# Optimization experiments

Measured on AMD Instinct MI355X. Metric: run time of the kernel, lower is better.

Reference implementation:

```python
import jax, jax.numpy as jnp
import numpy as np

THETA = 0.5  # forward default arg
ALPHA = 0.2  # LeakyReLU negative slope
NEG_INF = -9e15


def setup_inputs() -> dict:
    key = jax.random.key(0)
    k1, k2, k3, k4, k5 = jax.random.split(key, 5)
    N, F_IN, F_OUT = 8192, 256, 256
    h = jax.random.normal(k1, (N, F_IN), dtype=jnp.float32)
    adj = jax.random.randint(k2, (N, N), 0, 2, dtype=jnp.int32)
    cv_values = jax.random.uniform(k3, (N,), dtype=jnp.float32)
    # xavier_uniform with gain=1.414
    g = 1.414
    bw = g * np.sqrt(6.0 / (F_IN + F_OUT))
    W = jax.random.uniform(k4, (F_IN, F_OUT), dtype=jnp.float32, minval=-bw, maxval=bw)
    ba = g * np.sqrt(6.0 / (2 * F_OUT + 1))
    a = jax.random.uniform(k5, (2 * F_OUT, 1), dtype=jnp.float32, minval=-ba, maxval=ba)
    return {"h": h, "adj": adj, "cv_values": cv_values, "W": W, "a": a}


def reference(h, adj, cv_values, W, a):
    # Wh: [N, F_out]
    Wh = h @ W
    F_out = Wh.shape[1]
    a1 = a[:F_out, 0]   # [F_out]
    a2 = a[F_out:, 0]   # [F_out]
    # e_ij = LeakyReLU([Wh_i ; Wh_j] . a) = LeakyReLU(Wh_i.a1 + Wh_j.a2)
    f1 = Wh @ a1        # [N]
    f2 = Wh @ a2        # [N]
    e = jax.nn.leaky_relu(f1[:, None] + f2[None, :], negative_slope=ALPHA)
    # CV bias: theta * cv_i broadcast across row i
    e = e + THETA * cv_values[:, None]
    att = jnp.where(adj > 0, e, jnp.float32(NEG_INF))
    att = jax.nn.softmax(att, axis=1)
    # dropout is identity in eval mode (training=False)
    h_prime = att @ Wh  # [N, F_out]
    return jax.nn.elu(h_prime)  # concat=True branch
```

## Files before the change

kernel.cpp:

```cpp
#include <hip/hip_runtime.h>
#include <cstdint>
#include <cstddef>

typedef _Float16 half8 __attribute__((ext_vector_type(8)));
typedef _Float16 half4 __attribute__((ext_vector_type(4)));
typedef float f32x4 __attribute__((ext_vector_type(4)));
typedef int iv4 __attribute__((ext_vector_type(4)));

#define GAT_N 8192
#define GAT_F 256
#define GAT_NQ 8
#define GAT_ALPHA 0.2f
#define GAT_LOG2E 1.4426950408889634f

__device__ inline unsigned enc_f32(float x) {
    unsigned b = __float_as_uint(x);
    return (b & 0x80000000u) ? ~b : (b | 0x80000000u);
}
__device__ inline float dec_f32(unsigned u) {
    unsigned b = (u & 0x80000000u) ? (u ^ 0x80000000u) : ~u;
    return __uint_as_float(b);
}

__device__ inline unsigned pack8(iv4 v0, iv4 v1) {
    return (unsigned)(v0[0] > 0)        | ((unsigned)(v0[1] > 0) << 1)
         | ((unsigned)(v0[2] > 0) << 2) | ((unsigned)(v0[3] > 0) << 3)
         | ((unsigned)(v1[0] > 0) << 4) | ((unsigned)(v1[1] > 0) << 5)
         | ((unsigned)(v1[2] > 0) << 6) | ((unsigned)(v1[3] > 0) << 7);
}


__global__ __launch_bounds__(256) void gat_k0b_convert(
    const float* __restrict__ W, _Float16* __restrict__ WT,
    unsigned* __restrict__ f2mxEnc)
{
    const int g = blockIdx.x * 256 + threadIdx.x;
    if (g == 0) *f2mxEnc = 0u;
    const int k = g >> 8, n = g & 255;
    WT[n * GAT_F + k] = (_Float16)W[g];
}

__global__ __launch_bounds__(256, 2) void gat_k1_gemm(
    const float* __restrict__ h, const _Float16* __restrict__ WT,
    const float* __restrict__ a, _Float16* __restrict__ whT2,
    float* __restrict__ f1L, float* __restrict__ f2L,
    unsigned* __restrict__ f2mxEnc)
{
    __shared__ float sP1[4][16], sP2[4][16];
    const int wv = threadIdx.x >> 6;
    const int lane = threadIdx.x & 63;
    const int l15 = lane & 15;
    const int quad = lane >> 4;
    const int r0 = blockIdx.x * 16;

    f32x4 acc[4];
    #pragma unroll
    for (int t = 0; t < 4; ++t) { f32x4 z = {0.f,0.f,0.f,0.f}; acc[t] = z; }

    #pragma unroll
    for (int k0 = 0; k0 < GAT_F; k0 += 32) {
        const float* ap = h + (size_t)(r0 + l15) * GAT_F + k0 + quad * 8;
        const float4 a0 = *reinterpret_cast<const float4*>(ap);
        const float4 a1 = *reinterpret_cast<const float4*>(ap + 4);
        half8 af;
        af[0] = (_Float16)a0.x; af[1] = (_Float16)a0.y;
        af[2] = (_Float16)a0.z; af[3] = (_Float16)a0.w;
        af[4] = (_Float16)a1.x; af[5] = (_Float16)a1.y;
        af[6] = (_Float16)a1.z; af[7] = (_Float16)a1.w;
        #pragma unroll
        for (int t = 0; t < 4; ++t) {
            half8 bf = *reinterpret_cast<const half8*>(
                WT + (size_t)(wv * 64 + t * 16 + l15) * GAT_F + k0 + quad * 8);
            acc[t] = __builtin_amdgcn_mfma_f32_16x16x32_f16(af, bf, acc[t], 0, 0, 0);
        }
    }

    float p1[4] = {0.f,0.f,0.f,0.f}, p2[4] = {0.f,0.f,0.f,0.f};
    #pragma unroll
    for (int t = 0; t < 4; ++t) {
        float a1c = a[wv * 64 + t * 16 + l15];
        float a2c = a[GAT_F + wv * 64 + t * 16 + l15];
        #pragma unroll
        for (int r = 0; r < 4; ++r) {
            p1[r] = fmaf(acc[t][r], a1c, p1[r]);
            p2[r] = fmaf(acc[t][r], a2c, p2[r]);
        }
    }
    #pragma unroll
    for (int off = 1; off < 16; off <<= 1) {
        #pragma unroll
        for (int r = 0; r < 4; ++r) {
            p1[r] += __shfl_xor(p1[r], off);
            p2[r] += __shfl_xor(p2[r], off);
        }
    }
    if (l15 == 0) {
        #pragma unroll
        for (int r = 0; r < 4; ++r) {
            sP1[wv][quad * 4 + r] = p1[r];
            sP2[wv][quad * 4 + r] = p2[r];
        }
    }
    __syncthreads();
    if (threadIdx.x < 16) {
        const int row = threadIdx.x;
        const float s1 = (sP1[0][row] + sP1[1][row] + sP1[2][row] + sP1[3][row]) * GAT_LOG2E;
        const float s2 = (sP2[0][row] + sP2[1][row] + sP2[2][row] + sP2[3][row]) * GAT_LOG2E;
        f1L[r0 + row] = s1;
        f2L[r0 + row] = s2;
        float mx = s2;
        #pragma unroll
        for (int off = 1; off < 16; off <<= 1) mx = fmaxf(mx, __shfl_xor(mx, off));
        if (row == 0) atomicMax(f2mxEnc, enc_f32(mx));
    }

    const size_t tbase = (size_t)(r0 >> 6) * 16384
                       + (((r0 & 63) >> 3) + (quad >> 1)) * 2048
                       + (quad & 1) * 4;
    #pragma unroll
    for (int t = 0; t < 4; ++t) {
        const int c = wv * 64 + t * 16 + l15;
        half4 hv;
        #pragma unroll
        for (int r = 0; r < 4; ++r) hv[r] = (_Float16)acc[t][r];
        *reinterpret_cast<half4*>(whT2 + tbase + c * 8) = hv;
    }
}

__global__ __launch_bounds__(256, 2) void gat_k3_attn(
    const int* __restrict__ adj, const float* __restrict__ f1L,
    const float* __restrict__ f2L, const unsigned* __restrict__ f2mxEnc,
    const _Float16* __restrict__ whT2,
    _Float16* __restrict__ Ph,
    float* __restrict__ L)
{
    const int bx = blockIdx.x;
    const int q  = bx & 7;
    const int rb = bx >> 3;
    const int wv = threadIdx.x >> 6;
    const int lane = threadIdx.x & 63;
    const int l15 = lane & 15;
    const int quad = lane >> 4;

    const int kq = q * 1024;
    const int r0 = rb * 128 + wv * 32;
    const int rA = r0 + l15;
    const int rB = rA + 16;

    const float fmxL = dec_f32(*f2mxEnc);
    const float f1A = f1L[rA];
    const float f1B = f1L[rB];
    const float sA = f1A + fmxL;
    const float sBv = f1B + fmxL;
    const float CA = fmaxf(sA, GAT_ALPHA * sA);
    const float CB = fmaxf(sBv, GAT_ALPHA * sBv);
    const float uA = f1A - CA, vA = GAT_ALPHA * f1A - CA;
    const float uB = f1B - CB, vB = GAT_ALPHA * f1B - CB;

    f32x4 acc[2][16];
    #pragma unroll
    for (int s = 0; s < 2; ++s)
        #pragma unroll
        for (int t = 0; t < 16; ++t) {
            f32x4 z = {0.f,0.f,0.f,0.f};
            acc[s][t] = z;
        }
    float d0 = 0.f, d1 = 0.f;

    const int* aprA = adj + (size_t)rA * GAT_N + kq + quad * 8;
    const int* aprB = adj + (size_t)rB * GAT_N + kq + quad * 8;
    const float* f2q = f2L + kq + quad * 8;

    const _Float16* bfp0 = whT2 + (size_t)(q * 16) * 16384
                         + (size_t)quad * 2048 + (size_t)l15 * 8;

    iv4 xA0, xA1, xA2, xA3, xB0, xB1, xB2, xB3;
    #define ADJLOAD(s)                                                         \
        {                                                                      \
            const iv4* pa = reinterpret_cast<const iv4*>(aprA + (s) * 64);     \
            const iv4* pb = reinterpret_cast<const iv4*>(aprB + (s) * 64);     \
            xA0 = __builtin_nontemporal_load(pa);                              \
            xA1 = __builtin_nontemporal_load(pa + 1);                          \
            xA2 = __builtin_nontemporal_load(pa + 8);                          \
            xA3 = __builtin_nontemporal_load(pa + 9);                          \
            xB0 = __builtin_nontemporal_load(pb);                              \
            xB1 = __builtin_nontemporal_load(pb + 1);                          \
            xB2 = __builtin_nontemporal_load(pb + 8);                          \
            xB3 = __builtin_nontemporal_load(pb + 9);                          \
        }
    #define ADJPACK(ma, mb)                                                    \
        {                                                                      \
            ma = pack8(xA0, xA1) | (pack8(xA2, xA3) << 8);                     \
            mb = pack8(xB0, xB1) | (pack8(xB2, xB3) << 8);                     \
        }

    ADJLOAD(0)
    float4 nfa = *reinterpret_cast<const float4*>(f2q);
    float4 nfb = *reinterpret_cast<const float4*>(f2q + 4);
    unsigned cmA, cmB;
    ADJPACK(cmA, cmB)
    unsigned nmA = 0, nmB = 0;

    for (int step = 0; step < 16; ++step) {
        if (step < 15) ADJLOAD(step + 1)
        const _Float16* bstep = bfp0 + (size_t)step * 16384;

        #pragma unroll
        for (int k2 = 0; k2 < 2; ++k2) {
            const int u = step * 2 + k2;
            const float4 cfa = nfa, cfb = nfb;
            if (u < 31) {
                nfa = *reinterpret_cast<const float4*>(f2q + (u + 1) * 32);
                nfb = *reinterpret_cast<const float4*>(f2q + (u + 1) * 32 + 4);
            }
            const unsigned mA = (cmA >> (k2 * 8)) & 0xffu;
            const unsigned mB = (cmB >> (k2 * 8)) & 0xffu;
            const float f2v[8] = {cfa.x, cfa.y, cfa.z, cfa.w,
                                  cfb.x, cfb.y, cfb.z, cfb.w};
            float af2[8];
            #pragma unroll
            for (int j = 0; j < 8; ++j) af2[j] = GAT_ALPHA * f2v[j];

            half8 pA, pB;
            #pragma unroll
            for (int j = 0; j < 8; ++j) {
                float pa = __builtin_amdgcn_exp2f(fmaxf(uA + f2v[j], vA + af2[j]));
                pa = (mA & (1u << j)) ? pa : 0.f;
                d0 += pa;
                pA[j] = (_Float16)pa;
                float pb = __builtin_amdgcn_exp2f(fmaxf(uB + f2v[j], vB + af2[j]));
                pb = (mB & (1u << j)) ? pb : 0.f;
                d1 += pb;
                pB[j] = (_Float16)pb;
            }

            const _Float16* bk = bstep + k2 * 8192;
            #pragma unroll
            for (int t = 0; t < 16; ++t) {
                half8 bf = *reinterpret_cast<const half8*>(bk + t * 128);
                acc[0][t] = __builtin_amdgcn_mfma_f32_16x16x32_f16(pA, bf, acc[0][t], 0, 0, 0);
                acc[1][t] = __builtin_amdgcn_mfma_f32_16x16x32_f16(pB, bf, acc[1][t], 0, 0, 0);
            }
        }
        if (step < 15) ADJPACK(nmA, nmB)
        cmA = nmA; cmB = nmB;
    }
    #undef ADJLOAD
    #undef ADJPACK

    d0 += __shfl_xor(d0, 16); d0 += __shfl_xor(d0, 32);
    d1 += __shfl_xor(d1, 16); d1 += __shfl_xor(d1, 32);
    if (lane < 16) {
        float* Lq = L + q * GAT_N;
        Lq[rA] = d0; Lq[rB] = d1;
    }

    const int wid = rb * 4 + wv;
    _Float16* Pq = Ph + ((size_t)q * 256 + wid) * 8192;
    #pragma unroll
    for (int s = 0; s < 2; ++s)
        #pragma unroll
        for (int t = 0; t < 16; ++t) {
            half4 hv;
            #pragma unroll
            for (int r = 0; r < 4; ++r) hv[r] = (_Float16)acc[s][t][r];
            __builtin_nontemporal_store(hv,
                reinterpret_cast<half4*>(Pq + (size_t)(((s * 16 + t) * 64 + lane) * 4)));
        }
}

__global__ __launch_bounds__(256) void gat_k4_final(
    const _Float16* __restrict__ Ph, const float* __restrict__ L,
    float* __restrict__ out)
{
    const int tid = threadIdx.x;
    const int wid = blockIdx.x >> 3;
    __shared__ float s_rl[32];
    if (tid < 32) {
        const int row = wid * 32 + tid;
        float s = 0.f;
        #pragma unroll
        for (int q = 0; q < GAT_NQ; ++q) s += L[q * GAT_N + row];
        s_rl[tid] = 1.0f / fmaxf(s, 1e-30f);
    }
    __syncthreads();

    const int idx = blockIdx.x * 256 + tid;
    const int rem = idx & 2047;
    const int lane = rem & 63;
    const int st = rem >> 6;
    const int s = st >> 4, t = st & 15;
    const int l15 = lane & 15, quad = lane >> 4;
    const int lrow0 = s * 16 + quad * 4;
    const int col = t * 16 + l15;

    float accv[4] = {0.f, 0.f, 0.f, 0.f};
    #pragma unroll
    for (int q = 0; q < GAT_NQ; ++q) {
        half4 v = __builtin_nontemporal_load(reinterpret_cast<const half4*>(
            Ph + ((size_t)q * 256 + wid) * 8192 + (size_t)rem * 4));
        #pragma unroll
        for (int r = 0; r < 4; ++r) accv[r] += (float)v[r];
    }
    #pragma unroll
    for (int r = 0; r < 4; ++r) {
        const float v = accv[r] * s_rl[lrow0 + r];
        const float o = v > 0.f ? v : expm1f(v);
        __builtin_nontemporal_store(o,
            &out[(size_t)(wid * 32 + lrow0 + r) * GAT_F + col]);
    }
}

extern "C" void kernel_launch(void* const* d_in, const int* in_sizes, int n_in,
                              void* d_out, int out_size, void* d_ws, size_t ws_size,
                              hipStream_t stream)
{
    const float* h   = (const float*)d_in[0];
    const int*   adj = (const int*)d_in[1];
    const float* W   = (const float*)d_in[3];
    const float* a   = (const float*)d_in[4];
    float* out = (float*)d_out;
    char* ws = (char*)d_ws;

    const size_t SLAB = (size_t)GAT_N * GAT_F * 2;

    size_t off = 0;
    _Float16* whT2 = (_Float16*)(ws + off); off += SLAB;
    _Float16* Ph  = (_Float16*)(ws + off); off += GAT_NQ * SLAB;
    _Float16* WT  = (_Float16*)(ws + off); off += (size_t)GAT_F * GAT_F * 2;
    float* f1L = (float*)(ws + off); off += GAT_N * 4;
    float* f2L = (float*)(ws + off); off += GAT_N * 4;
    float* L   = (float*)(ws + off); off += GAT_NQ * GAT_N * 4;
    unsigned* f2mxEnc = (unsigned*)(ws + off); off += 256;

    gat_k0b_convert<<<256, 256, 0, stream>>>(W, WT, f2mxEnc);
    gat_k1_gemm<<<512, 256, 0, stream>>>(h, WT, a, whT2, f1L, f2L, f2mxEnc);
    gat_k3_attn<<<512, 256, 0, stream>>>(adj, f1L, f2L, f2mxEnc, whT2, Ph, L);
    gat_k4_final<<<2048, 256, 0, stream>>>(Ph, L, out);
}
```

Baseline: 470.5 us.

## Stage Wh tiles through double-buffered LDS and cache f2 slice in shared memory

The attention kernel now cooperatively loads each step's 32 KB fp16 Wh tile from global memory into a double-buffered LDS array. It overlaps the next tile's global load with the current step's MFMA work, and the four waves read B fragments from LDS instead of each fetching them from global/L2. The f2 slice for the block is cached in LDS, and MFMA sections get raised wave priority via s_setprio. Nontemporal hints are dropped in the reduction kernel. The cost is 64 KB+ of LDS per block, which may cut occupancy below the 2 blocks requested by launch bounds, plus a __syncthreads each step.

```diff
diff --git a/kernel.cpp b/kernel.cpp
--- a/kernel.cpp
+++ b/kernel.cpp
@@ -134,6 +134,9 @@
     _Float16* __restrict__ Ph,
     float* __restrict__ L)
 {
+    __shared__ __align__(16) _Float16 sB[2][16384];
+    __shared__ __align__(16) float sF2[1024];
+
     const int bx = blockIdx.x;
     const int q  = bx & 7;
     const int rb = bx >> 3;
@@ -150,13 +153,18 @@
     const float fmxL = dec_f32(*f2mxEnc);
     const float f1A = f1L[rA];
     const float f1B = f1L[rB];
-    const float sA = f1A + fmxL;
+    const float sAv = f1A + fmxL;
     const float sBv = f1B + fmxL;
-    const float CA = fmaxf(sA, GAT_ALPHA * sA);
+    const float CA = fmaxf(sAv, GAT_ALPHA * sAv);
     const float CB = fmaxf(sBv, GAT_ALPHA * sBv);
     const float uA = f1A - CA, vA = GAT_ALPHA * f1A - CA;
     const float uB = f1B - CB, vB = GAT_ALPHA * f1B - CB;
 
+    {
+        const float4 v = *reinterpret_cast<const float4*>(f2L + kq + threadIdx.x * 4);
+        *reinterpret_cast<float4*>(&sF2[threadIdx.x * 4]) = v;
+    }
+
     f32x4 acc[2][16];
     #pragma unroll
     for (int s = 0; s < 2; ++s)
@@ -169,10 +177,6 @@
 
     const int* aprA = adj + (size_t)rA * GAT_N + kq + quad * 8;
     const int* aprB = adj + (size_t)rB * GAT_N + kq + quad * 8;
-    const float* f2q = f2L + kq + quad * 8;
-
-    const _Float16* bfp0 = whT2 + (size_t)(q * 16) * 16384
-                         + (size_t)quad * 2048 + (size_t)l15 * 8;
 
     iv4 xA0, xA1, xA2, xA3, xB0, xB1, xB2, xB3;
     #define ADJLOAD(s)                                                         \
@@ -194,57 +198,106 @@
             mb = pack8(xB0, xB1) | (pack8(xB2, xB3) << 8);                     \
         }
 
+    const _Float16* tile0 = whT2 + (size_t)(q * 16) * 16384
+                          + (size_t)wv * 4096 + (size_t)lane * 8;
+    _Float16* const lbase0 = &sB[0][wv * 4096 + lane * 8];
+    int4 g0, g1, g2, g3, g4, g5, g6, g7;
+    #define STAGE_LOAD(step)                                                   \
+        {                                                                      \
+            const _Float16* gp = tile0 + (size_t)(step) * 16384;               \
+            g0 = *reinterpret_cast<const int4*>(gp);                           \
+            g1 = *reinterpret_cast<const int4*>(gp + 512);                     \
+            g2 = *reinterpret_cast<const int4*>(gp + 1024);                    \
+            g3 = *reinterpret_cast<const int4*>(gp + 1536);                    \
+            g4 = *reinterpret_cast<const int4*>(gp + 2048);                    \
+            g5 = *reinterpret_cast<const int4*>(gp + 2560);                    \
+            g6 = *reinterpret_cast<const int4*>(gp + 3072);                    \
+            g7 = *reinterpret_cast<const int4*>(gp + 3584);                    \
+        }
+    #define STAGE_WRITE(buf)                                                   \
+        {                                                                      \
+            _Float16* lp = lbase0 + (buf) * 16384;                             \
+            *reinterpret_cast<int4*>(lp)        = g0;                          \
+            *reinterpret_cast<int4*>(lp + 512)  = g1;                          \
+            *reinterpret_cast<int4*>(lp + 1024) = g2;                          \
+            *reinterpret_cast<int4*>(lp + 1536) = g3;                          \
+            *reinterpret_cast<int4*>(lp + 2048) = g4;                          \
+            *reinterpret_cast<int4*>(lp + 2560) = g5;                          \
+            *reinterpret_cast<int4*>(lp + 3072) = g6;                          \
+            *reinterpret_cast<int4*>(lp + 3584) = g7;                          \
+        }
+
+    unsigned cmA, cmB, nmA, nmB;
+    const _Float16* const sflat = &sB[0][0];
+
+    #define STEP_COMPUTE(cur, step)                                            \
+        {                                                                      \
+            _Pragma("unroll")                                                  \
+            for (int k2 = 0; k2 < 2; ++k2) {                                   \
+                const float* fp = &sF2[(step) * 64 + k2 * 32 + quad * 8];      \
+                const float4 cfa = *reinterpret_cast<const float4*>(fp);       \
+                const float4 cfb = *reinterpret_cast<const float4*>(fp + 4);   \
+                const unsigned mA = (cmA >> (k2 * 8)) & 0xffu;                 \
+                const unsigned mB = (cmB >> (k2 * 8)) & 0xffu;                 \
+                const float f2v[8] = {cfa.x, cfa.y, cfa.z, cfa.w,              \
+                                      cfb.x, cfb.y, cfb.z, cfb.w};             \
+                float af2[8];                                                  \
+                _Pragma("unroll")                                              \
+                for (int j = 0; j < 8; ++j) af2[j] = GAT_ALPHA * f2v[j];       \
+                half8 pA, pB;                                                  \
+                _Pragma("unroll")                                              \
+                for (int j = 0; j < 8; ++j) {                                  \
+                    float pa = __builtin_amdgcn_exp2f(                         \
+                        fmaxf(uA + f2v[j], vA + af2[j]));                      \
+                    pa = (mA & (1u << j)) ? pa : 0.f;                          \
+                    d0 += pa;                                                  \
+                    pA[j] = (_Float16)pa;                                      \
+                    float pb = __builtin_amdgcn_exp2f(                         \
+                        fmaxf(uB + f2v[j], vB + af2[j]));                      \
+                    pb = (mB & (1u << j)) ? pb : 0.f;                          \
+                    d1 += pb;                                                  \
+                    pB[j] = (_Float16)pb;                                      \
+                }                                                              \
+                const _Float16* bk = sflat + (cur) * 16384                     \
+                                   + (k2 * 4 + quad) * 2048 + l15 * 8;         \
+                __builtin_amdgcn_s_setprio(1);                                 \
+                _Pragma("unroll")                                              \
+                for (int t = 0; t < 16; ++t) {                                 \
+                    half8 bf = *reinterpret_cast<const half8*>(bk + t * 128);  \
+                    acc[0][t] = __builtin_amdgcn_mfma_f32_16x16x32_f16(        \
+                        pA, bf, acc[0][t], 0, 0, 0);                           \
+                    acc[1][t] = __builtin_amdgcn_mfma_f32_16x16x32_f16(        \
+                        pB, bf, acc[1][t], 0, 0, 0);                           \
+                }                                                              \
+                __builtin_amdgcn_s_setprio(0);                                 \
+            }                                                                  \
+        }
+
+    STAGE_LOAD(0)
     ADJLOAD(0)
-    float4 nfa = *reinterpret_cast<const float4*>(f2q);
-    float4 nfb = *reinterpret_cast<const float4*>(f2q + 4);
-    unsigned cmA, cmB;
+    STAGE_WRITE(0)
     ADJPACK(cmA, cmB)
-    unsigned nmA = 0, nmB = 0;
+    __syncthreads();
 
     for (int step = 0; step < 16; ++step) {
-        if (step < 15) ADJLOAD(step + 1)
-        const _Float16* bstep = bfp0 + (size_t)step * 16384;
-
-        #pragma unroll
-        for (int k2 = 0; k2 < 2; ++k2) {
-            const int u = step * 2 + k2;
-            const float4 cfa = nfa, cfb = nfb;
-            if (u < 31) {
-                nfa = *reinterpret_cast<const float4*>(f2q + (u + 1) * 32);
-                nfb = *reinterpret_cast<const float4*>(f2q + (u + 1) * 32 + 4);
-            }
-            const unsigned mA = (cmA >> (k2 * 8)) & 0xffu;
-            const unsigned mB = (cmB >> (k2 * 8)) & 0xffu;
-            const float f2v[8] = {cfa.x, cfa.y, cfa.z, cfa.w,
-                                  cfb.x, cfb.y, cfb.z, cfb.w};
-            float af2[8];
-            #pragma unroll
-            for (int j = 0; j < 8; ++j) af2[j] = GAT_ALPHA * f2v[j];
-
-            half8 pA, pB;
-            #pragma unroll
-            for (int j = 0; j < 8; ++j) {
-                float pa = __builtin_amdgcn_exp2f(fmaxf(uA + f2v[j], vA + af2[j]));
-                pa = (mA & (1u << j)) ? pa : 0.f;
-                d0 += pa;
-                pA[j] = (_Float16)pa;
-                float pb = __builtin_amdgcn_exp2f(fmaxf(uB + f2v[j], vB + af2[j]));
-                pb = (mB & (1u << j)) ? pb : 0.f;
-                d1 += pb;
-                pB[j] = (_Float16)pb;
-            }
-
-            const _Float16* bk = bstep + k2 * 8192;
-            #pragma unroll
-            for (int t = 0; t < 16; ++t) {
-                half8 bf = *reinterpret_cast<const half8*>(bk + t * 128);
-                acc[0][t] = __builtin_amdgcn_mfma_f32_16x16x32_f16(pA, bf, acc[0][t], 0, 0, 0);
-                acc[1][t] = __builtin_amdgcn_mfma_f32_16x16x32_f16(pB, bf, acc[1][t], 0, 0, 0);
-            }
-        }
-        if (step < 15) ADJPACK(nmA, nmB)
-        cmA = nmA; cmB = nmB;
-    }
+        const int cur = step & 1;
+        if (step < 15) {
+            STAGE_LOAD(step + 1)
+            ADJLOAD(step + 1)
+        }
+
+        STEP_COMPUTE(cur, step)
+
+        if (step < 15) {
+            STAGE_WRITE(1 - cur)
+            ADJPACK(nmA, nmB)
+            cmA = nmA; cmB = nmB;
+            __syncthreads();
+        }
+    }
+    #undef STAGE_LOAD
+    #undef STAGE_WRITE
+    #undef STEP_COMPUTE
     #undef ADJLOAD
     #undef ADJPACK
 
@@ -297,8 +350,8 @@
     float accv[4] = {0.f, 0.f, 0.f, 0.f};
     #pragma unroll
     for (int q = 0; q < GAT_NQ; ++q) {
-        half4 v = __builtin_nontemporal_load(reinterpret_cast<const half4*>(
-            Ph + ((size_t)q * 256 + wid) * 8192 + (size_t)rem * 4));
+        half4 v = *reinterpret_cast<const half4*>(
+            Ph + ((size_t)q * 256 + wid) * 8192 + (size_t)rem * 4);
         #pragma unroll
         for (int r = 0; r < 4; ++r) accv[r] += (float)v[r];
     }
@@ -306,8 +359,7 @@
     for (int r = 0; r < 4; ++r) {
         const float v = accv[r] * s_rl[lrow0 + r];
         const float o = v > 0.f ? v : expm1f(v);
-        __builtin_nontemporal_store(o,
-            &out[(size_t)(wid * 32 + lrow0 + r) * GAT_F + col]);
+        out[(size_t)(wid * 32 + lrow0 + r) * GAT_F + col] = o;
     }
 }
 
```

After: 607.2 us. +29.0%, slower.

## Stage Wh tiles in LDS with async double buffering, halve rows per wave

Applied to the files above, without the earlier changes.

The attention kernel now loads each 32-column K-slice of Wh into shared memory through global_load_lds into a double buffer, and all four waves share it instead of each reading B fragments from global memory. Each wave now handles 16 rows instead of 32, so the grid doubles to 1024 blocks. Launch bounds rise to 4 blocks per CU, and f2 values are cached in LDS. The intent is less redundant global B traffic and higher occupancy, at the cost of a barrier every step and half the MFMA reuse per B fragment. The final reduction kernel and the partial-result layout are adjusted to match the 16-row tiles, and the adj loads drop their nontemporal hint.

```diff
diff --git a/kernel.cpp b/kernel.cpp
--- a/kernel.cpp
+++ b/kernel.cpp
@@ -127,13 +127,16 @@
     }
 }
 
-__global__ __launch_bounds__(256, 2) void gat_k3_attn(
+__global__ __launch_bounds__(256, 4) void gat_k3_attn(
     const int* __restrict__ adj, const float* __restrict__ f1L,
     const float* __restrict__ f2L, const unsigned* __restrict__ f2mxEnc,
     const _Float16* __restrict__ whT2,
     _Float16* __restrict__ Ph,
     float* __restrict__ L)
 {
+    __shared__ __align__(16) _Float16 sB[2][8192];
+    __shared__ __align__(16) float sF2[1024];
+
     const int bx = blockIdx.x;
     const int q  = bx & 7;
     const int rb = bx >> 3;
@@ -143,130 +146,115 @@
     const int quad = lane >> 4;
 
     const int kq = q * 1024;
-    const int r0 = rb * 128 + wv * 32;
+    const int r0 = rb * 64 + wv * 16;
     const int rA = r0 + l15;
-    const int rB = rA + 16;
 
     const float fmxL = dec_f32(*f2mxEnc);
     const float f1A = f1L[rA];
-    const float f1B = f1L[rB];
-    const float sA = f1A + fmxL;
-    const float sBv = f1B + fmxL;
-    const float CA = fmaxf(sA, GAT_ALPHA * sA);
-    const float CB = fmaxf(sBv, GAT_ALPHA * sBv);
+    const float sAv = f1A + fmxL;
+    const float CA = fmaxf(sAv, GAT_ALPHA * sAv);
     const float uA = f1A - CA, vA = GAT_ALPHA * f1A - CA;
-    const float uB = f1B - CB, vB = GAT_ALPHA * f1B - CB;
-
-    f32x4 acc[2][16];
-    #pragma unroll
-    for (int s = 0; s < 2; ++s)
-        #pragma unroll
-        for (int t = 0; t < 16; ++t) {
-            f32x4 z = {0.f,0.f,0.f,0.f};
-            acc[s][t] = z;
-        }
-    float d0 = 0.f, d1 = 0.f;
+
+    {
+        const float4 v = *reinterpret_cast<const float4*>(f2L + kq + threadIdx.x * 4);
+        *reinterpret_cast<float4*>(&sF2[threadIdx.x * 4]) = v;
+    }
+
+    f32x4 acc[16];
+    #pragma unroll
+    for (int t = 0; t < 16; ++t) { f32x4 z = {0.f,0.f,0.f,0.f}; acc[t] = z; }
+    float d0 = 0.f;
 
     const int* aprA = adj + (size_t)rA * GAT_N + kq + quad * 8;
-    const int* aprB = adj + (size_t)rB * GAT_N + kq + quad * 8;
-    const float* f2q = f2L + kq + quad * 8;
-
-    const _Float16* bfp0 = whT2 + (size_t)(q * 16) * 16384
-                         + (size_t)quad * 2048 + (size_t)l15 * 8;
-
-    iv4 xA0, xA1, xA2, xA3, xB0, xB1, xB2, xB3;
+
+    iv4 xA0, xA1;
     #define ADJLOAD(s)                                                         \
         {                                                                      \
-            const iv4* pa = reinterpret_cast<const iv4*>(aprA + (s) * 64);     \
-            const iv4* pb = reinterpret_cast<const iv4*>(aprB + (s) * 64);     \
-            xA0 = __builtin_nontemporal_load(pa);                              \
-            xA1 = __builtin_nontemporal_load(pa + 1);                          \
-            xA2 = __builtin_nontemporal_load(pa + 8);                          \
-            xA3 = __builtin_nontemporal_load(pa + 9);                          \
-            xB0 = __builtin_nontemporal_load(pb);                              \
-            xB1 = __builtin_nontemporal_load(pb + 1);                          \
-            xB2 = __builtin_nontemporal_load(pb + 8);                          \
-            xB3 = __builtin_nontemporal_load(pb + 9);                          \
-        }
-    #define ADJPACK(ma, mb)                                                    \
+            const int* pa = aprA + (s) * 32;                                   \
+            xA0 = *reinterpret_cast<const iv4*>(pa);                           \
+            xA1 = *reinterpret_cast<const iv4*>(pa + 4);                       \
+        }
+    #define ADJPACK(m) { m = pack8(xA0, xA1); }
+
+    const _Float16* tile0 = whT2 + (size_t)(q * 32) * 8192
+                          + wv * 2048 + (size_t)lane * 8;
+    #define STAGE(buf, step)                                                   \
         {                                                                      \
-            ma = pack8(xA0, xA1) | (pack8(xA2, xA3) << 8);                     \
-            mb = pack8(xB0, xB1) | (pack8(xB2, xB3) << 8);                     \
-        }
-
+            _Pragma("unroll")                                                  \
+            for (int i = 0; i < 4; ++i) {                                      \
+                const _Float16* gp = tile0 + (size_t)(step) * 8192 + i * 512;  \
+                _Float16* lp = &sB[buf][wv * 2048 + i * 512];                  \
+                __builtin_amdgcn_global_load_lds(                              \
+                    (const __attribute__((address_space(1))) void*)gp,         \
+                    (__attribute__((address_space(3))) void*)lp, 16, 0, 0);    \
+            }                                                                  \
+        }
+
+    unsigned cmA, nmA;
     ADJLOAD(0)
-    float4 nfa = *reinterpret_cast<const float4*>(f2q);
-    float4 nfb = *reinterpret_cast<const float4*>(f2q + 4);
-    unsigned cmA, cmB;
-    ADJPACK(cmA, cmB)
-    unsigned nmA = 0, nmB = 0;
-
-    for (int step = 0; step < 16; ++step) {
-        if (step < 15) ADJLOAD(step + 1)
-        const _Float16* bstep = bfp0 + (size_t)step * 16384;
-
-        #pragma unroll
-        for (int k2 = 0; k2 < 2; ++k2) {
-            const int u = step * 2 + k2;
-            const float4 cfa = nfa, cfb = nfb;
-            if (u < 31) {
-                nfa = *reinterpret_cast<const float4*>(f2q + (u + 1) * 32);
-                nfb = *reinterpret_cast<const float4*>(f2q + (u + 1) * 32 + 4);
-            }
-            const unsigned mA = (cmA >> (k2 * 8)) & 0xffu;
-            const unsigned mB = (cmB >> (k2 * 8)) & 0xffu;
-            const float f2v[8] = {cfa.x, cfa.y, cfa.z, cfa.w,
-                                  cfb.x, cfb.y, cfb.z, cfb.w};
-            float af2[8];
-            #pragma unroll
-            for (int j = 0; j < 8; ++j) af2[j] = GAT_ALPHA * f2v[j];
-
-            half8 pA, pB;
-            #pragma unroll
-            for (int j = 0; j < 8; ++j) {
-                float pa = __builtin_amdgcn_exp2f(fmaxf(uA + f2v[j], vA + af2[j]));
-                pa = (mA & (1u << j)) ? pa : 0.f;
-                d0 += pa;
-                pA[j] = (_Float16)pa;
-                float pb = __builtin_amdgcn_exp2f(fmaxf(uB + f2v[j], vB + af2[j]));
-                pb = (mB & (1u << j)) ? pb : 0.f;
-                d1 += pb;
-                pB[j] = (_Float16)pb;
-            }
-
-            const _Float16* bk = bstep + k2 * 8192;
-            #pragma unroll
-            for (int t = 0; t < 16; ++t) {
-                half8 bf = *reinterpret_cast<const half8*>(bk + t * 128);
-                acc[0][t] = __builtin_amdgcn_mfma_f32_16x16x32_f16(pA, bf, acc[0][t], 0, 0, 0);
-                acc[1][t] = __builtin_amdgcn_mfma_f32_16x16x32_f16(pB, bf, acc[1][t], 0, 0, 0);
-            }
-        }
-        if (step < 15) ADJPACK(nmA, nmB)
-        cmA = nmA; cmB = nmB;
-    }
+    STAGE(0, 0)
+    ADJPACK(cmA)
+    __syncthreads();
+
+    const _Float16* const sflat = &sB[0][0];
+
+    for (int step = 0; step < 32; ++step) {
+        const int cur = step & 1;
+        if (step < 31) {
+            ADJLOAD(step + 1)
+            STAGE(1 - cur, step + 1)
+        }
+
+        const float* fp = &sF2[step * 32 + quad * 8];
+        const float4 cfa = *reinterpret_cast<const float4*>(fp);
+        const float4 cfb = *reinterpret_cast<const float4*>(fp + 4);
+        const float f2v[8] = {cfa.x, cfa.y, cfa.z, cfa.w,
+                              cfb.x, cfb.y, cfb.z, cfb.w};
+        float af2[8];
+        #pragma unroll
+        for (int j = 0; j < 8; ++j) af2[j] = GAT_ALPHA * f2v[j];
+
+        half8 pA;
+        #pragma unroll
+        for (int j = 0; j < 8; ++j) {
+            float pa = __builtin_amdgcn_exp2f(fmaxf(uA + f2v[j], vA + af2[j]));
+            pa = (cmA & (1u << j)) ? pa : 0.f;
+            d0 += pa;
+            pA[j] = (_Float16)pa;
+        }
+
+        const _Float16* bk = sflat + cur * 8192 + quad * 2048 + l15 * 8;
+        __builtin_amdgcn_s_setprio(1);
+        #pragma unroll
+        for (int t = 0; t < 16; ++t) {
+            half8 bf = *reinterpret_cast<const half8*>(bk + t * 128);
+            acc[t] = __builtin_amdgcn_mfma_f32_16x16x32_f16(pA, bf, acc[t], 0, 0, 0);
+        }
+        __builtin_amdgcn_s_setprio(0);
+
+        if (step < 31) {
+            ADJPACK(nmA)
+            cmA = nmA;
+            __syncthreads();
+        }
+    }
+    #undef STAGE
     #undef ADJLOAD
     #undef ADJPACK
 
     d0 += __shfl_xor(d0, 16); d0 += __shfl_xor(d0, 32);
-    d1 += __shfl_xor(d1, 16); d1 += __shfl_xor(d1, 32);
-    if (lane < 16) {
-        float* Lq = L + q * GAT_N;
-        Lq[rA] = d0; Lq[rB] = d1;
-    }
+    if (lane < 16) L[q * GAT_N + rA] = d0;
 
     const int wid = rb * 4 + wv;
-    _Float16* Pq = Ph + ((size_t)q * 256 + wid) * 8192;
-    #pragma unroll
-    for (int s = 0; s < 2; ++s)
-        #pragma unroll
-        for (int t = 0; t < 16; ++t) {
-            half4 hv;
-            #pragma unroll
-            for (int r = 0; r < 4; ++r) hv[r] = (_Float16)acc[s][t][r];
-            __builtin_nontemporal_store(hv,
-                reinterpret_cast<half4*>(Pq + (size_t)(((s * 16 + t) * 64 + lane) * 4)));
-        }
+    _Float16* Pq = Ph + ((size_t)q * 512 + wid) * 4096;
+    #pragma unroll
+    for (int t = 0; t < 16; ++t) {
+        half4 hv;
+        #pragma unroll
+        for (int r = 0; r < 4; ++r) hv[r] = (_Float16)acc[t][r];
+        __builtin_nontemporal_store(hv,
+            reinterpret_cast<half4*>(Pq + (size_t)((t * 64 + lane) * 4)));
+    }
 }
 
 __global__ __launch_bounds__(256) void gat_k4_final(
@@ -274,10 +262,10 @@
     float* __restrict__ out)
 {
     const int tid = threadIdx.x;
-    const int wid = blockIdx.x >> 3;
-    __shared__ float s_rl[32];
-    if (tid < 32) {
-        const int row = wid * 32 + tid;
+    const int wid = blockIdx.x >> 2;
+    __shared__ float s_rl[16];
+    if (tid < 16) {
+        const int row = wid * 16 + tid;
         float s = 0.f;
         #pragma unroll
         for (int q = 0; q < GAT_NQ; ++q) s += L[q * GAT_N + row];
@@ -286,19 +274,18 @@
     __syncthreads();
 
     const int idx = blockIdx.x * 256 + tid;
-    const int rem = idx & 2047;
+    const int rem = idx & 1023;
     const int lane = rem & 63;
-    const int st = rem >> 6;
-    const int s = st >> 4, t = st & 15;
+    const int t = rem >> 6;
     const int l15 = lane & 15, quad = lane >> 4;
-    const int lrow0 = s * 16 + quad * 4;
+    const int lrow0 = quad * 4;
     const int col = t * 16 + l15;
 
     float accv[4] = {0.f, 0.f, 0.f, 0.f};
     #pragma unroll
     for (int q = 0; q < GAT_NQ; ++q) {
-        half4 v = __builtin_nontemporal_load(reinterpret_cast<const half4*>(
-            Ph + ((size_t)q * 256 + wid) * 8192 + (size_t)rem * 4));
+        half4 v = *reinterpret_cast<const half4*>(
+            Ph + ((size_t)q * 512 + wid) * 4096 + (size_t)rem * 4);
         #pragma unroll
         for (int r = 0; r < 4; ++r) accv[r] += (float)v[r];
     }
@@ -306,8 +293,7 @@
     for (int r = 0; r < 4; ++r) {
         const float v = accv[r] * s_rl[lrow0 + r];
         const float o = v > 0.f ? v : expm1f(v);
-        __builtin_nontemporal_store(o,
-            &out[(size_t)(wid * 32 + lrow0 + r) * GAT_F + col]);
+        out[(size_t)(wid * 16 + lrow0 + r) * GAT_F + col] = o;
     }
 }
 
@@ -335,6 +321,6 @@
 
     gat_k0b_convert<<<256, 256, 0, stream>>>(W, WT, f2mxEnc);
     gat_k1_gemm<<<512, 256, 0, stream>>>(h, WT, a, whT2, f1L, f2L, f2mxEnc);
-    gat_k3_attn<<<512, 256, 0, stream>>>(adj, f1L, f2L, f2mxEnc, whT2, Ph, L);
+    gat_k3_attn<<<1024, 256, 0, stream>>>(adj, f1L, f2L, f2mxEnc, whT2, Ph, L);
     gat_k4_final<<<2048, 256, 0, stream>>>(Ph, L, out);
 }
```

Result: faster. 433.8 us (-7.8%).
